# Performance work log

Hardware: AMD Instinct MI355X
Metric: run time of the kernel (lower is better)

## Reference

```python
import jax, jax.numpy as jnp
import numpy as np

EPS = 1e-12

def _normalize(v):
    n = jnp.linalg.norm(v, axis=-1, keepdims=True)
    return v / jnp.maximum(n, EPS)

def _bgs(J):
    # J: [b, N, D, 3, 2] -> rotation matrices R [b, N, D, 3, 3]
    b1 = _normalize(J[..., :, 0])
    a2 = J[..., :, 1]
    dot = jnp.sum(b1 * a2, axis=-1, keepdims=True)
    b2 = _normalize(a2 - dot * b1)
    b3 = jnp.cross(b1, b2)
    return jnp.stack([b1, b2, b3], axis=-1)  # columns b1,b2,b3

def setup_inputs() -> dict:
    key = jax.random.key(0)
    k1, k2, k3, k4, k5 = jax.random.split(key, 5)
    B, N, D, OUT = 16, 4096, 64, 64
    X = jax.random.normal(k1, (B, N, D, 3), dtype=jnp.float32)
    J = jax.random.normal(k2, (B, N, D, 3, 2), dtype=jnp.float32)
    A = jax.random.normal(k3, (OUT, D), dtype=jnp.float32)
    Bm = jax.random.normal(k4, (OUT, D), dtype=jnp.float32)
    C = jax.random.normal(k5, (OUT, D), dtype=jnp.float32)
    return {"X": X, "J": J, "A": A, "Bm": Bm, "C": C}

def reference(X, J, A, Bm, C):
    R = _bgs(J)  # [b, N, D, 3, 3]
    # RT_i . X == column i of R dotted with X -> scalar per channel
    RTX = jnp.einsum('bndij,bndi->bndj', R, X)  # [b, N, D, 3], j-th entry = RT_j X
    rt0 = RTX[..., 0:1]
    rt1 = RTX[..., 1:2]
    rt2 = RTX[..., 2:3]
    col0 = R[..., :, 0]
    col1 = R[..., :, 1]
    col2 = R[..., :, 2]
    # a_term (after adding b_term, as in original forward)
    a_term = col1 * rt1 + col2 * rt2 + col2 * rt1 - col1 * rt2  # [b, N, D, 3]
    c_term = col0 * rt0
    Y = jnp.einsum('fe,bnei->bnfi', A, a_term) + jnp.einsum('fe,bnei->bnfi', C, c_term)
    Y = jnp.einsum('fe,bnei->bnfi', Bm, Y)
    return Y
```

## Files before the change

### kernel.cpp

```cpp
#include <hip/hip_runtime.h>


typedef __bf16 bf16x8 __attribute__((ext_vector_type(8)));
typedef float floatx4 __attribute__((ext_vector_type(4)));

#define ZRS  68
#define WLDS 816

__global__ __launch_bounds__(64) void prep_kernel(const float* __restrict__ A,
                                                  const float* __restrict__ Bm,
                                                  const float* __restrict__ C,
                                                  __bf16* __restrict__ acat) {
    int tid = blockIdx.x * 64 + threadIdx.x;
    int f = tid >> 6;
    int e = tid & 63;
    float m = 0.f, m2 = 0.f;
    #pragma unroll 8
    for (int k = 0; k < 64; ++k) {
        float b = Bm[f * 64 + k];
        m  = fmaf(b, A[k * 64 + e], m);
        m2 = fmaf(b, C[k * 64 + e], m2);
    }
    acat[f * 128 + 2 * e]     = (__bf16)m;
    acat[f * 128 + 2 * e + 1] = (__bf16)m2;
}

static __device__ __forceinline__ unsigned pk(float a, float c) {
    unsigned short ua = __builtin_bit_cast(unsigned short, (__bf16)a);
    unsigned short uc = __builtin_bit_cast(unsigned short, (__bf16)c);
    return ((unsigned)uc << 16) | ua;
}

__global__ __launch_bounds__(256, 4) void main_kernel(const float* __restrict__ X,
                                                      const float* __restrict__ J,
                                                      const __bf16* __restrict__ acat,
                                                      float* __restrict__ out) {
    __shared__ __align__(16) float lds[4096 + 4 * WLDS];

    const int tid  = threadIdx.x;
    const int wave = tid >> 6;
    const int lane = tid & 63;
    const int l15  = lane & 15;
    const int quad = lane >> 4;
    const int pbase = blockIdx.x * 16 + wave * 4;

    float2 jreg[4][3];
    float  xreg[4][3];
    {
        const float* Jb = J + (size_t)pbase * 384 + lane * 6;
        const float* Xb = X + (size_t)pbase * 192 + lane * 3;
        #pragma unroll
        for (int pi = 0; pi < 4; ++pi) {
            jreg[pi][0] = *(const float2*)(Jb + pi * 384);
            jreg[pi][1] = *(const float2*)(Jb + pi * 384 + 2);
            jreg[pi][2] = *(const float2*)(Jb + pi * 384 + 4);
            xreg[pi][0] = Xb[pi * 192];
            xreg[pi][1] = Xb[pi * 192 + 1];
            xreg[pi][2] = Xb[pi * 192 + 2];
        }
    }

    {
        const floatx4* ag = (const floatx4*)acat;
        floatx4 t[4];
        #pragma unroll
        for (int u = 0; u < 4; ++u) t[u] = ag[u * 256 + tid];
        #pragma unroll
        for (int u = 0; u < 4; ++u) {
            int Ld  = (u * 256 + tid) * 4;
            int row = Ld >> 6;
            int dst = Ld ^ ((row & 7) << 2);
            *(floatx4*)(lds + dst) = t[u];
        }
    }
    __syncthreads();

    float* zbase = lds + 4096 + wave * WLDS;

    #pragma unroll
    for (int pi = 0; pi < 4; ++pi) {
        float a0x = jreg[pi][0].x, a1x = jreg[pi][0].y;
        float a0y = jreg[pi][1].x, a1y = jreg[pi][1].y;
        float a0z = jreg[pi][2].x, a1z = jreg[pi][2].y;
        float xx = xreg[pi][0], xy = xreg[pi][1], xz = xreg[pi][2];

        float n0 = sqrtf(a0x * a0x + a0y * a0y + a0z * a0z);
        float r0 = 1.0f / fmaxf(n0, 1e-12f);
        float b1x = a0x * r0, b1y = a0y * r0, b1z = a0z * r0;

        float d  = b1x * a1x + b1y * a1y + b1z * a1z;
        float ux = a1x - d * b1x, uy = a1y - d * b1y, uz = a1z - d * b1z;
        float n2 = sqrtf(ux * ux + uy * uy + uz * uz);
        float r2 = 1.0f / fmaxf(n2, 1e-12f);
        float b2x = ux * r2, b2y = uy * r2, b2z = uz * r2;

        float b3x = b1y * b2z - b1z * b2y;
        float b3y = b1z * b2x - b1x * b2z;
        float b3z = b1x * b2y - b1y * b2x;

        float rt0 = b1x * xx + b1y * xy + b1z * xz;
        float rt1 = b2x * xx + b2y * xy + b2z * xz;
        float rt2 = b3x * xx + b3y * xy + b3z * xz;

        float s = rt1 - rt2, tt = rt1 + rt2;

        unsigned* zr = (unsigned*)zbase + pi * (3 * ZRS);
        zr[lane]           = pk(b2x * s + b3x * tt, b1x * rt0);
        zr[ZRS + lane]     = pk(b2y * s + b3y * tt, b1y * rt0);
        zr[2 * ZRS + lane] = pk(b2z * s + b3z * tt, b1z * rt0);
    }

    __asm__ volatile("s_waitcnt lgkmcnt(0)" ::: "memory");

    floatx4 acc[4];
    #pragma unroll
    for (int mt = 0; mt < 4; ++mt) acc[mt] = (floatx4){0.f, 0.f, 0.f, 0.f};

    int row = l15 > 11 ? 11 : l15;
    int pz  = (row * 21846) >> 16;
    int iz  = row - pz * 3;
    const __bf16* zb = (const __bf16*)zbase + pz * (3 * ZRS * 2) + iz * (ZRS * 2);
    const int sw = (l15 & 7) << 2;
    #pragma unroll
    for (int kc = 0; kc < 4; ++kc) {
        bf16x8 b = *(const bf16x8*)(zb + kc * 32 + quad * 8);
        #pragma unroll
        for (int mt = 0; mt < 4; ++mt) {
            int r   = mt * 16 + l15;
            int off = r * 64 + ((kc * 16 + quad * 4) ^ sw);
            bf16x8 a = *(const bf16x8*)((const __bf16*)lds + off * 2);
            acc[mt] = __builtin_amdgcn_mfma_f32_16x16x32_bf16(a, b, acc[mt], 0, 0, 0);
        }
    }

    __asm__ volatile("s_waitcnt lgkmcnt(0)" ::: "memory");

    float* dl = zbase;
    #pragma unroll
    for (int mt = 0; mt < 4; ++mt) {
        int n = l15;
        if (n < 12) {
            int pl = (n * 21846) >> 16;
            int i  = n - pl * 3;
            float* dst = dl + pl * 196 + i;
            #pragma unroll
            for (int r = 0; r < 4; ++r) {
                int f = mt * 16 + quad * 4 + r;
                dst[f * 3] = acc[mt][r];
            }
        }
    }

    __asm__ volatile("s_waitcnt lgkmcnt(0)" ::: "memory");

    floatx4* og = (floatx4*)(out + (size_t)pbase * 192);
    #pragma unroll
    for (int t = 0; t < 3; ++t) {
        int g  = t * 64 + lane;
        int pg = (g * 1366) >> 16;
        int o  = g - pg * 48;
        og[g] = *(const floatx4*)(dl + pg * 196 + o * 4);
    }
}

extern "C" void kernel_launch(void* const* d_in, const int* in_sizes, int n_in,
                              void* d_out, int out_size, void* d_ws, size_t ws_size,
                              hipStream_t stream) {
    const float* X  = (const float*)d_in[0];
    const float* J  = (const float*)d_in[1];
    const float* A  = (const float*)d_in[2];
    const float* Bm = (const float*)d_in[3];
    const float* C  = (const float*)d_in[4];
    float* out = (float*)d_out;
    __bf16* acat = (__bf16*)d_ws;

    prep_kernel<<<64, 64, 0, stream>>>(A, Bm, C, acat);

    main_kernel<<<4096, 256, 0, stream>>>(X, J, acat, out);
}
```

Baseline: 204.8 us.

## Pre-pack weight matrix in MFMA fragment order and merge LDS barriers

The prep kernel now writes the fused bf16 weight matrix directly in the per-lane MFMA A-fragment order. The main kernel can then copy it linearly into LDS and read each fragment with one contiguous 16-byte access per lane, with no XOR-swizzle address math. The weight global loads are issued before the J/X loads. The separate barrier after the weight copy is folded into a single __syncthreads after the Z writes, and the explicit s_waitcnt asm lines are dropped. Launch bounds go from 4 to 5 blocks per CU, which trades register budget for occupancy and relies on in-wave LDS ordering for the later scratch reuse.

```diff
diff --git a/kernel.cpp b/kernel.cpp
--- a/kernel.cpp
+++ b/kernel.cpp
@@ -21,8 +21,14 @@
         m  = fmaf(b, A[k * 64 + e], m);
         m2 = fmaf(b, C[k * 64 + e], m2);
     }
-    acat[f * 128 + 2 * e]     = (__bf16)m;
-    acat[f * 128 + 2 * e + 1] = (__bf16)m2;
+    int mt  = f >> 4, l15 = f & 15;
+    int k1  = 2 * e;
+    int kc  = k1 >> 5;
+    int qd  = (k1 >> 3) & 3;
+    int j   = k1 & 7;
+    int p   = ((mt * 4 + kc) * 64 + qd * 16 + l15) * 8 + j;
+    acat[p]     = (__bf16)m;
+    acat[p + 1] = (__bf16)m2;
 }
 
 static __device__ __forceinline__ unsigned pk(float a, float c) {
@@ -31,7 +37,7 @@
     return ((unsigned)uc << 16) | ua;
 }
 
-__global__ __launch_bounds__(256, 4) void main_kernel(const float* __restrict__ X,
+__global__ __launch_bounds__(256, 5) void main_kernel(const float* __restrict__ X,
                                                       const float* __restrict__ J,
                                                       const __bf16* __restrict__ acat,
                                                       float* __restrict__ out) {
@@ -43,6 +49,12 @@
     const int l15  = lane & 15;
     const int quad = lane >> 4;
     const int pbase = blockIdx.x * 16 + wave * 4;
+
+    const floatx4* ag = (const floatx4*)acat;
+    floatx4 t0 = ag[tid];
+    floatx4 t1 = ag[256 + tid];
+    floatx4 t2 = ag[512 + tid];
+    floatx4 t3 = ag[768 + tid];
 
     float2 jreg[4][3];
     float  xreg[4][3];
@@ -61,19 +73,12 @@
     }
 
     {
-        const floatx4* ag = (const floatx4*)acat;
-        floatx4 t[4];
-        #pragma unroll
-        for (int u = 0; u < 4; ++u) t[u] = ag[u * 256 + tid];
-        #pragma unroll
-        for (int u = 0; u < 4; ++u) {
-            int Ld  = (u * 256 + tid) * 4;
-            int row = Ld >> 6;
-            int dst = Ld ^ ((row & 7) << 2);
-            *(floatx4*)(lds + dst) = t[u];
-        }
+        floatx4* al = (floatx4*)lds;
+        al[tid]       = t0;
+        al[256 + tid] = t1;
+        al[512 + tid] = t2;
+        al[768 + tid] = t3;
     }
-    __syncthreads();
 
     float* zbase = lds + 4096 + wave * WLDS;
 
@@ -110,7 +115,7 @@
         zr[2 * ZRS + lane] = pk(b2z * s + b3z * tt, b1z * rt0);
     }
 
-    __asm__ volatile("s_waitcnt lgkmcnt(0)" ::: "memory");
+    __syncthreads();
 
     floatx4 acc[4];
     #pragma unroll
@@ -119,21 +124,17 @@
     int row = l15 > 11 ? 11 : l15;
     int pz  = (row * 21846) >> 16;
     int iz  = row - pz * 3;
-    const __bf16* zb = (const __bf16*)zbase + pz * (3 * ZRS * 2) + iz * (ZRS * 2);
-    const int sw = (l15 & 7) << 2;
+    const __bf16* zb   = (const __bf16*)zbase + pz * (3 * ZRS * 2) + iz * (ZRS * 2);
+    const __bf16* albf = (const __bf16*)lds;
     #pragma unroll
     for (int kc = 0; kc < 4; ++kc) {
         bf16x8 b = *(const bf16x8*)(zb + kc * 32 + quad * 8);
         #pragma unroll
         for (int mt = 0; mt < 4; ++mt) {
-            int r   = mt * 16 + l15;
-            int off = r * 64 + ((kc * 16 + quad * 4) ^ sw);
-            bf16x8 a = *(const bf16x8*)((const __bf16*)lds + off * 2);
+            bf16x8 a = *(const bf16x8*)(albf + ((mt * 4 + kc) * 64 + lane) * 8);
             acc[mt] = __builtin_amdgcn_mfma_f32_16x16x32_bf16(a, b, acc[mt], 0, 0, 0);
         }
     }
-
-    __asm__ volatile("s_waitcnt lgkmcnt(0)" ::: "memory");
 
     float* dl = zbase;
     #pragma unroll
@@ -150,8 +151,6 @@
             }
         }
     }
-
-    __asm__ volatile("s_waitcnt lgkmcnt(0)" ::: "memory");
 
     floatx4* og = (floatx4*)(out + (size_t)pbase * 192);
     #pragma unroll
```

After: 205.7 us. No clear change (+0.4%).
